# Optimization experiments

Measured on AMD Instinct MI355X. Metric: run time of the kernel, lower is better.

Reference implementation:

```python
import jax, jax.numpy as jnp
import numpy as np

N_NODES = 100000
N_EDGES = 1600000
D_IN = 128
D_OUT = 128


def setup_inputs() -> dict:
    key = jax.random.key(0)
    k1, k2, k3, k4, k5, k6 = jax.random.split(key, 6)
    x = jax.random.normal(k1, (N_NODES, D_IN), dtype=jnp.float32)
    edge_src = jax.random.randint(k2, (N_EDGES,), 0, N_NODES, dtype=jnp.int64 if jax.config.jax_enable_x64 else jnp.int32)
    edge_dst = jax.random.randint(k3, (N_EDGES,), 0, N_NODES, dtype=jnp.int64 if jax.config.jax_enable_x64 else jnp.int32)
    edge_val = jax.random.uniform(k4, (N_EDGES,), dtype=jnp.float32)
    # nn.Linear(2*D_IN, D_OUT): store W as [2*D_IN, D_OUT] (transposed torch layout)
    W = jax.random.normal(k5, (2 * D_IN, D_OUT), dtype=jnp.float32) * (1.0 / np.sqrt(2 * D_IN))
    b = jax.random.normal(k6, (D_OUT,), dtype=jnp.float32) * 0.01
    return {"x": x, "edge_src": edge_src, "edge_dst": edge_dst, "edge_val": edge_val, "W": W, "b": b}


def reference(x, edge_src, edge_dst, edge_val, W, b):
    # support = adj @ x  (sparse COO: adj[dst, src] = edge_val)
    gathered = x[edge_src] * edge_val[:, None]               # [E, D_IN]
    support = jax.ops.segment_sum(gathered, edge_dst, num_segments=x.shape[0])  # [N, D_IN]
    # concat self + aggregated neighbor features, then linear
    h = jnp.concatenate([x, support], axis=1)                # [N, 2*D_IN]
    return h @ W + b                                          # [N, D_OUT]
```

## Files before the change

### kernel.cpp

```cpp
#include <hip/hip_runtime.h>

#define D 128
#define BN 64
#define NBIN 391
#define NBMAX 512
#define CHUNK 4096
#define SCAP 12

typedef __attribute__((ext_vector_type(8))) short bf16x8;
typedef __attribute__((ext_vector_type(4))) float f32x4;

__device__ __forceinline__ unsigned short f2bf(float f) {
    unsigned int u = __builtin_bit_cast(unsigned int, f);
    u = (u + 0x7fffu + ((u >> 16) & 1u)) >> 16;
    return (unsigned short)u;
}
__device__ __forceinline__ float bf2f(unsigned int u) {
    return __builtin_bit_cast(float, u << 16);
}

__global__ void prep_kernel(const float* __restrict__ x,
                            unsigned short* __restrict__ x_bf,
                            const float* __restrict__ W,
                            unsigned short* __restrict__ WT,
                            const int* __restrict__ edst,
                            int* __restrict__ hcnt,
                            int n4, int XB, int WB, int E, int NCH) {
    __shared__ int h[NBMAX];
    int blk = blockIdx.x, tid = threadIdx.x;
    if (blk < XB) {
        int i = blk * 256 + tid;
        if (i < n4) {
            float4 v = ((const float4*)x)[i];
            ushort4 s;
            s.x = f2bf(v.x); s.y = f2bf(v.y); s.z = f2bf(v.z); s.w = f2bf(v.w);
            ((ushort4*)x_bf)[i] = s;
        }
    } else if (blk < XB + WB) {
        int t = (blk - XB) * 256 + tid;
        if (t < 2 * D * D) {
            int col = t & 127, k = t >> 7;
            WT[col * 256 + k] = f2bf(W[k * D + col]);
        }
    } else {
        int c = blk - XB - WB;
        h[tid] = 0; h[tid + 256] = 0;
        __syncthreads();
        int base = c * CHUNK;
        int n = min(CHUNK, E - base);
#pragma unroll
        for (int k = 0; k < 16; ++k) {
            int li = k * 256 + tid;
            if (li < n) atomicAdd(&h[edst[base + li] >> 8], 1);
        }
        __syncthreads();
        hcnt[tid * NCH + c]         = h[tid];
        hcnt[(tid + 256) * NCH + c] = h[tid + 256];
    }
}

__global__ __launch_bounds__(256) void binscan_kernel(const int* __restrict__ hcnt,
                                                      int* __restrict__ cpos,
                                                      int* __restrict__ ccnt, int NCH) {
    const int tid = threadIdx.x;
    const int lane = tid & 63;
    const int b = blockIdx.x * 4 + (tid >> 6);
    int run = 0;
    for (int c0 = 0; c0 < NCH; c0 += 64) {
        int c = c0 + lane;
        int v = (c < NCH) ? hcnt[b * NCH + c] : 0;
        int s = v;
#pragma unroll
        for (int off = 1; off < 64; off <<= 1) {
            int u = __shfl_up(s, off, 64);
            if (lane >= off) s += u;
        }
        if (c < NCH) cpos[c * NBMAX + b] = run + s - v;
        run += __shfl(s, 63, 64);
    }
    if (lane == 0) ccnt[b] = run;
}

__global__ __launch_bounds__(512) void cfill_kernel(const int* __restrict__ esrc,
                                                    const int* __restrict__ edst,
                                                    const float* __restrict__ eval,
                                                    const int* __restrict__ ccnt,
                                                    const int* __restrict__ cpos,
                                                    int2* __restrict__ ep, int E, int NCH) {
    __shared__ int lh[NBMAX];
    __shared__ int lcur[NBMAX];
    __shared__ int cbs[NBMAX];
    __shared__ int wsum[16];
    __shared__ int2 ord[CHUNK];
    __shared__ unsigned short obk[CHUNK];

    const int t = threadIdx.x;
    const int w = t >> 6, lane = t & 63;
    const int blk = blockIdx.x;
    const int base = blk * CHUNK;
    const int n = min(CHUNK, E - base);

    lh[t] = 0;
    __syncthreads();

    int esv[8]; int ebk[8];
    float evv[8];
#pragma unroll
    for (int k = 0; k < 8; ++k) {
        int li = k * 512 + t;
        if (li < n) {
            int i = base + li;
            int dst = edst[i];
            esv[k] = esrc[i];
            evv[k] = eval[i];
            int b = dst >> 8;
            ebk[k] = b | ((dst & 255) << 16);
            atomicAdd(&lh[b], 1);
        } else ebk[k] = -1;
    }
    __syncthreads();

    {
        int v1 = lh[t], v2 = ccnt[t];
        int s1 = v1, s2 = v2;
#pragma unroll
        for (int off = 1; off < 64; off <<= 1) {
            int u1 = __shfl_up(s1, off, 64);
            int u2 = __shfl_up(s2, off, 64);
            if (lane >= off) { s1 += u1; s2 += u2; }
        }
        if (lane == 63) { wsum[w] = s1; wsum[8 + w] = s2; }
        __syncthreads();
        if (w == 0) {
            int x1 = (lane < 8) ? wsum[lane] : 0;
            int x2 = (lane < 8) ? wsum[8 + lane] : 0;
            int y1 = x1, y2 = x2;
#pragma unroll
            for (int off = 1; off < 8; off <<= 1) {
                int u1 = __shfl_up(y1, off, 64);
                int u2 = __shfl_up(y2, off, 64);
                if (lane >= off) { y1 += u1; y2 += u2; }
            }
            if (lane < 8) { wsum[lane] = y1 - x1; wsum[8 + lane] = y2 - x2; }
        }
        __syncthreads();
        lcur[t] = s1 - v1 + wsum[w];
        cbs[t]  = s2 - v2 + wsum[8 + w];
    }
    __syncthreads();

#pragma unroll
    for (int k = 0; k < 8; ++k) {
        if (ebk[k] >= 0) {
            int b = ebk[k] & 0xffff, nl = ebk[k] >> 16;
            int slot = atomicAdd(&lcur[b], 1);
            ord[slot] = make_int2((esv[k] << 8) | nl, __builtin_bit_cast(int, evv[k]));
            obk[slot] = (unsigned short)b;
        }
    }
    __syncthreads();

    if (t < NBIN) {
        int c2 = lh[t];
        if (c2) lh[t] = cbs[t] + cpos[blk * NBMAX + t] - (lcur[t] - c2);
    }
    __syncthreads();

    for (int i = t; i < n; i += 512) {
        int b = obk[i];
        ep[lh[b] + i] = ord[i];
    }
}

__global__ __launch_bounds__(512) void csort_kernel(int2* __restrict__ ep,
                                                    const int* __restrict__ ccnt,
                                                    int* __restrict__ node_start) {
    __shared__ int h[256];
    __shared__ int cbs[NBMAX];
    __shared__ int wsum[8];

    const int t = threadIdx.x;
    const int w = t >> 6, lane = t & 63;
    const int bin = blockIdx.x;

    if (t < 256) h[t] = 0;
    {
        int v = ccnt[t];
        int s = v;
#pragma unroll
        for (int off = 1; off < 64; off <<= 1) {
            int u = __shfl_up(s, off, 64);
            if (lane >= off) s += u;
        }
        if (lane == 63) wsum[w] = s;
        __syncthreads();
        if (w == 0) {
            int x = (lane < 8) ? wsum[lane] : 0;
            int y = x;
#pragma unroll
            for (int off = 1; off < 8; off <<= 1) {
                int u = __shfl_up(y, off, 64);
                if (lane >= off) y += u;
            }
            if (lane < 8) wsum[lane] = y - x;
        }
        __syncthreads();
        cbs[t] = s - v + wsum[w];
    }
    __syncthreads();

    const int cb = cbs[bin];
    const int ce = cb + ccnt[bin];

    int2 ev[SCAP];
#pragma unroll
    for (int k = 0; k < SCAP; ++k) {
        int idx = cb + k * 512 + t;
        if (idx < ce) {
            int2 e = ep[idx];
            ev[k] = e;
            atomicAdd(&h[e.x & 255], 1);
        } else ev[k] = make_int2(-1, 0);
    }
    __syncthreads();

    {
        int v = (t < 256) ? h[t] : 0;
        int s = v;
#pragma unroll
        for (int off = 1; off < 64; off <<= 1) {
            int u = __shfl_up(s, off, 64);
            if (lane >= off) s += u;
        }
        if (lane == 63) wsum[w] = s;
        __syncthreads();
        if (w == 0) {
            int x = (lane < 8) ? wsum[lane] : 0;
            int y = x;
#pragma unroll
            for (int off = 1; off < 8; off <<= 1) {
                int u = __shfl_up(y, off, 64);
                if (lane >= off) y += u;
            }
            if (lane < 8) wsum[lane] = y - x;
        }
        __syncthreads();
        if (t < 256) {
            int st = cb + s - v + wsum[w];
            node_start[bin * 256 + t] = st;
            h[t] = st;
        }
    }
    __syncthreads();

#pragma unroll
    for (int k = 0; k < SCAP; ++k) {
        if (ev[k].x >= 0) {
            int nl = ev[k].x & 255;
            int pos = atomicAdd(&h[nl], 1);
            ep[pos] = make_int2(ev[k].x & 0xFFFFFF3F, ev[k].y);
        }
    }
}

__global__ __launch_bounds__(256, 8) void gather_fused_kernel(
        const unsigned short* __restrict__ x_bf,
        const int* __restrict__ node_start,
        const int2* __restrict__ edge_pack,
        const unsigned short* __restrict__ WT,
        const float* __restrict__ bias,
        float* __restrict__ out, int N) {
    __shared__ unsigned short accb[BN * 136];
    __shared__ int nb[BN + 1];

    const int tid = threadIdx.x;
    const int node0 = blockIdx.x * BN;
    const int w = tid >> 6, lane = tid & 63;
    unsigned int* accw = (unsigned int*)accb;

    for (int i = tid * 8; i < BN * 136; i += 2048)
        *(uint4*)(accb + i) = make_uint4(0u, 0u, 0u, 0u);
    if (tid <= BN) nb[tid] = node_start[node0 + tid];
    __syncthreads();

    const int js = __builtin_amdgcn_readfirstlane(nb[w * 16]);
    const int je = __builtin_amdgcn_readfirstlane(nb[w * 16 + 16]);
    const unsigned short* xl = x_bf + lane * 2;

    int cur = -1;
    float ax = 0.f, ay = 0.f;
    for (int g = js; g < je; g += 16) {
        int m = je - g; if (m > 16) m = 16;
        int2 e[16];
#pragma unroll
        for (int k = 0; k < 16; ++k) {
            int idx = g + k; if (idx >= je) idx = je - 1;
            e[k] = edge_pack[idx];
        }
        unsigned int p[16];
#pragma unroll
        for (int k = 0; k < 16; ++k)
            p[k] = *(const unsigned int*)(xl + ((e[k].x >> 8) << 7));
#pragma unroll
        for (int k = 0; k < 16; ++k) {
            if (k < m) {
                int nd = e[k].x & 63;
                if (nd != cur) {
                    if (cur >= 0)
                        accw[cur * 68 + lane] =
                            (unsigned int)f2bf(ax) | ((unsigned int)f2bf(ay) << 16);
                    cur = nd; ax = 0.f; ay = 0.f;
                }
                float v = __builtin_bit_cast(float, e[k].y);
                ax += bf2f(p[k] & 0xffffu) * v;
                ay += bf2f(p[k] >> 16) * v;
            }
        }
    }
    if (cur >= 0)
        accw[cur * 68 + lane] = (unsigned int)f2bf(ax) | ((unsigned int)f2bf(ay) << 16);
    __syncthreads();

    const int quad = lane >> 4;
    const int l15  = lane & 15;
    const int colbase = w * 32;

    f32x4 acc[4][2];
#pragma unroll
    for (int rt = 0; rt < 4; ++rt) {
        acc[rt][0] = (f32x4){0.f, 0.f, 0.f, 0.f};
        acc[rt][1] = (f32x4){0.f, 0.f, 0.f, 0.f};
    }

#pragma unroll
    for (int ks = 0; ks < 8; ++ks) {
        bf16x8 wf0 = *(const bf16x8*)(WT + (size_t)(colbase + l15) * 256 + ks * 32 + quad * 8);
        bf16x8 wf1 = *(const bf16x8*)(WT + (size_t)(colbase + 16 + l15) * 256 + ks * 32 + quad * 8);
#pragma unroll
        for (int rt = 0; rt < 4; ++rt) {
            int row = rt * 16 + l15;
            bf16x8 a;
            if (ks < 4) {
                int rg = node0 + row; if (rg >= N) rg = N - 1;
                a = *(const bf16x8*)(x_bf + (size_t)rg * D + ks * 32 + quad * 8);
            } else {
                a = *(const bf16x8*)(accb + row * 136 + (ks - 4) * 32 + quad * 8);
            }
            acc[rt][0] = __builtin_amdgcn_mfma_f32_16x16x32_bf16(a, wf0, acc[rt][0], 0, 0, 0);
            acc[rt][1] = __builtin_amdgcn_mfma_f32_16x16x32_bf16(a, wf1, acc[rt][1], 0, 0, 0);
        }
    }

#pragma unroll
    for (int ct = 0; ct < 2; ++ct) {
        int col = colbase + ct * 16 + l15;
        float bv = bias[col];
#pragma unroll
        for (int rt = 0; rt < 4; ++rt) {
#pragma unroll
            for (int rg = 0; rg < 4; ++rg) {
                int row = node0 + rt * 16 + quad * 4 + rg;
                if (row < N)
                    out[(size_t)row * D + col] = acc[rt][ct][rg] + bv;
            }
        }
    }
}

extern "C" void kernel_launch(void* const* d_in, const int* in_sizes, int n_in,
                              void* d_out, int out_size, void* d_ws, size_t ws_size,
                              hipStream_t stream) {
    const float* x    = (const float*)d_in[0];
    const int*   esrc = (const int*)d_in[1];
    const int*   edst = (const int*)d_in[2];
    const float* eval = (const float*)d_in[3];
    const float* W    = (const float*)d_in[4];
    const float* bias = (const float*)d_in[5];
    float*       out  = (float*)d_out;

    const int N  = in_sizes[0] / D;
    const int E  = in_sizes[1];
    const int NG  = (N + BN - 1) / BN;
    const int NCH = (E + CHUNK - 1) / CHUNK;

    char* ws = (char*)d_ws;
    unsigned short* x_bf  = (unsigned short*)ws;
    int2*           ep    = (int2*)(ws + 25600000);
    int*            hcnt  = (int*)(ws + 25600000);
    unsigned short* WT    = (unsigned short*)(ws + 38400000);
    int*            nbg   = (int*)(ws + 38465536);
    int*            ccnt  = (int*)(ws + 38865920);
    int*            cpos  = (int*)(ws + 38870016);

    const int n4 = N * D / 4;
    const int XB = (n4 + 255) / 256;
    const int WB = (2 * D * D + 255) / 256;

    prep_kernel<<<XB + WB + NCH, 256, 0, stream>>>(x, x_bf, W, WT, edst, hcnt,
                                                   n4, XB, WB, E, NCH);
    binscan_kernel<<<128, 256, 0, stream>>>(hcnt, cpos, ccnt, NCH);
    cfill_kernel<<<NCH, 512, 0, stream>>>(esrc, edst, eval, ccnt, cpos, ep, E, NCH);
    csort_kernel<<<NBIN, 512, 0, stream>>>(ep, ccnt, nbg);
    gather_fused_kernel<<<NG, 256, 0, stream>>>(x_bf, nbg, ep, WT, bias, out, N);
    (void)ws_size; (void)n_in; (void)out_size;
}
```

Before: 239.9 us.

## Use 64-node buckets and sort within buckets in gather kernel LDS

Changes the destination bucketing from 256-node bins to 64-node buckets matching the gather block size. The separate csort pass, which re-read and re-wrote the edge array globally, is removed. Each gather block now loads its bucket's edges, counting-sorts them by node in shared memory, and accumulates from LDS. Histogram and offset arrays shrink to 16-bit, and a small single-block kernel scans the bucket counts. This risks dropping edges if a bucket exceeds the 1536 capacity, and adds LDS pressure to the gather kernel.

```diff
diff --git a/kernel.cpp b/kernel.cpp
--- a/kernel.cpp
+++ b/kernel.cpp
@@ -2,10 +2,10 @@
 
 #define D 128
 #define BN 64
-#define NBIN 391
-#define NBMAX 512
+#define NBKT 1563
+#define NBMAX 2048
 #define CHUNK 4096
-#define SCAP 12
+#define GCAP 1536
 
 typedef __attribute__((ext_vector_type(8))) short bf16x8;
 typedef __attribute__((ext_vector_type(4))) float f32x4;
@@ -24,7 +24,7 @@
                             const float* __restrict__ W,
                             unsigned short* __restrict__ WT,
                             const int* __restrict__ edst,
-                            int* __restrict__ hcnt,
+                            unsigned short* __restrict__ hcnt,
                             int n4, int XB, int WB, int E, int NCH) {
     __shared__ int h[NBMAX];
     int blk = blockIdx.x, tid = threadIdx.x;
@@ -44,23 +44,27 @@
         }
     } else {
         int c = blk - XB - WB;
-        h[tid] = 0; h[tid + 256] = 0;
+#pragma unroll
+        for (int j = 0; j < 8; ++j) h[tid + j * 256] = 0;
         __syncthreads();
         int base = c * CHUNK;
         int n = min(CHUNK, E - base);
 #pragma unroll
         for (int k = 0; k < 16; ++k) {
             int li = k * 256 + tid;
-            if (li < n) atomicAdd(&h[edst[base + li] >> 8], 1);
-        }
-        __syncthreads();
-        hcnt[tid * NCH + c]         = h[tid];
-        hcnt[(tid + 256) * NCH + c] = h[tid + 256];
-    }
-}
-
-__global__ __launch_bounds__(256) void binscan_kernel(const int* __restrict__ hcnt,
-                                                      int* __restrict__ cpos,
+            if (li < n) atomicAdd(&h[edst[base + li] >> 6], 1);
+        }
+        __syncthreads();
+#pragma unroll
+        for (int j = 0; j < 8; ++j) {
+            int b = tid + j * 256;
+            hcnt[(size_t)b * NCH + c] = (unsigned short)h[b];
+        }
+    }
+}
+
+__global__ __launch_bounds__(256) void binscan_kernel(const unsigned short* __restrict__ hcnt,
+                                                      unsigned short* __restrict__ cpos,
                                                       int* __restrict__ ccnt, int NCH) {
     const int tid = threadIdx.x;
     const int lane = tid & 63;
@@ -68,29 +72,49 @@
     int run = 0;
     for (int c0 = 0; c0 < NCH; c0 += 64) {
         int c = c0 + lane;
-        int v = (c < NCH) ? hcnt[b * NCH + c] : 0;
+        int v = (c < NCH) ? (int)hcnt[(size_t)b * NCH + c] : 0;
         int s = v;
 #pragma unroll
         for (int off = 1; off < 64; off <<= 1) {
             int u = __shfl_up(s, off, 64);
             if (lane >= off) s += u;
         }
-        if (c < NCH) cpos[c * NBMAX + b] = run + s - v;
+        if (c < NCH) cpos[(size_t)c * NBMAX + b] = (unsigned short)(run + s - v);
         run += __shfl(s, 63, 64);
     }
     if (lane == 0) ccnt[b] = run;
+}
+
+__global__ __launch_bounds__(256) void cscan_kernel(const int* __restrict__ ccnt,
+                                                    int* __restrict__ cbase) {
+    __shared__ int p[256];
+    int t = threadIdx.x;
+    int c[8]; int loc = 0;
+#pragma unroll
+    for (int k = 0; k < 8; ++k) { c[k] = ccnt[t * 8 + k]; loc += c[k]; }
+    p[t] = loc;
+    __syncthreads();
+    for (int off = 1; off < 256; off <<= 1) {
+        int v = p[t];
+        int u = (t >= off) ? p[t - off] : 0;
+        __syncthreads();
+        p[t] = v + u;
+        __syncthreads();
+    }
+    int ex = p[t] - loc;
+#pragma unroll
+    for (int k = 0; k < 8; ++k) { cbase[t * 8 + k] = ex; ex += c[k]; }
 }
 
 __global__ __launch_bounds__(512) void cfill_kernel(const int* __restrict__ esrc,
                                                     const int* __restrict__ edst,
                                                     const float* __restrict__ eval,
-                                                    const int* __restrict__ ccnt,
-                                                    const int* __restrict__ cpos,
-                                                    int2* __restrict__ ep, int E, int NCH) {
+                                                    const int* __restrict__ cbase,
+                                                    const unsigned short* __restrict__ cpos,
+                                                    int2* __restrict__ ep, int E) {
     __shared__ int lh[NBMAX];
     __shared__ int lcur[NBMAX];
-    __shared__ int cbs[NBMAX];
-    __shared__ int wsum[16];
+    __shared__ int wsum[8];
     __shared__ int2 ord[CHUNK];
     __shared__ unsigned short obk[CHUNK];
 
@@ -100,7 +124,8 @@
     const int base = blk * CHUNK;
     const int n = min(CHUNK, E - base);
 
-    lh[t] = 0;
+#pragma unroll
+    for (int j = 0; j < 4; ++j) lh[t + j * 512] = 0;
     __syncthreads();
 
     int esv[8]; int ebk[8];
@@ -113,79 +138,16 @@
             int dst = edst[i];
             esv[k] = esrc[i];
             evv[k] = eval[i];
-            int b = dst >> 8;
-            ebk[k] = b | ((dst & 255) << 16);
+            int b = dst >> 6;
+            ebk[k] = b | ((dst & 63) << 16);
             atomicAdd(&lh[b], 1);
         } else ebk[k] = -1;
     }
     __syncthreads();
 
     {
-        int v1 = lh[t], v2 = ccnt[t];
-        int s1 = v1, s2 = v2;
-#pragma unroll
-        for (int off = 1; off < 64; off <<= 1) {
-            int u1 = __shfl_up(s1, off, 64);
-            int u2 = __shfl_up(s2, off, 64);
-            if (lane >= off) { s1 += u1; s2 += u2; }
-        }
-        if (lane == 63) { wsum[w] = s1; wsum[8 + w] = s2; }
-        __syncthreads();
-        if (w == 0) {
-            int x1 = (lane < 8) ? wsum[lane] : 0;
-            int x2 = (lane < 8) ? wsum[8 + lane] : 0;
-            int y1 = x1, y2 = x2;
-#pragma unroll
-            for (int off = 1; off < 8; off <<= 1) {
-                int u1 = __shfl_up(y1, off, 64);
-                int u2 = __shfl_up(y2, off, 64);
-                if (lane >= off) { y1 += u1; y2 += u2; }
-            }
-            if (lane < 8) { wsum[lane] = y1 - x1; wsum[8 + lane] = y2 - x2; }
-        }
-        __syncthreads();
-        lcur[t] = s1 - v1 + wsum[w];
-        cbs[t]  = s2 - v2 + wsum[8 + w];
-    }
-    __syncthreads();
-
-#pragma unroll
-    for (int k = 0; k < 8; ++k) {
-        if (ebk[k] >= 0) {
-            int b = ebk[k] & 0xffff, nl = ebk[k] >> 16;
-            int slot = atomicAdd(&lcur[b], 1);
-            ord[slot] = make_int2((esv[k] << 8) | nl, __builtin_bit_cast(int, evv[k]));
-            obk[slot] = (unsigned short)b;
-        }
-    }
-    __syncthreads();
-
-    if (t < NBIN) {
-        int c2 = lh[t];
-        if (c2) lh[t] = cbs[t] + cpos[blk * NBMAX + t] - (lcur[t] - c2);
-    }
-    __syncthreads();
-
-    for (int i = t; i < n; i += 512) {
-        int b = obk[i];
-        ep[lh[b] + i] = ord[i];
-    }
-}
-
-__global__ __launch_bounds__(512) void csort_kernel(int2* __restrict__ ep,
-                                                    const int* __restrict__ ccnt,
-                                                    int* __restrict__ node_start) {
-    __shared__ int h[256];
-    __shared__ int cbs[NBMAX];
-    __shared__ int wsum[8];
-
-    const int t = threadIdx.x;
-    const int w = t >> 6, lane = t & 63;
-    const int bin = blockIdx.x;
-
-    if (t < 256) h[t] = 0;
-    {
-        int v = ccnt[t];
+        int c0 = lh[4 * t], c1 = lh[4 * t + 1], c2 = lh[4 * t + 2], c3 = lh[4 * t + 3];
+        int v = c0 + c1 + c2 + c3;
         int s = v;
 #pragma unroll
         for (int off = 1; off < 64; off <<= 1) {
@@ -205,86 +167,100 @@
             if (lane < 8) wsum[lane] = y - x;
         }
         __syncthreads();
-        cbs[t] = s - v + wsum[w];
-    }
-    __syncthreads();
-
-    const int cb = cbs[bin];
-    const int ce = cb + ccnt[bin];
-
-    int2 ev[SCAP];
-#pragma unroll
-    for (int k = 0; k < SCAP; ++k) {
-        int idx = cb + k * 512 + t;
-        if (idx < ce) {
-            int2 e = ep[idx];
-            ev[k] = e;
-            atomicAdd(&h[e.x & 255], 1);
-        } else ev[k] = make_int2(-1, 0);
-    }
-    __syncthreads();
-
-    {
-        int v = (t < 256) ? h[t] : 0;
-        int s = v;
-#pragma unroll
-        for (int off = 1; off < 64; off <<= 1) {
-            int u = __shfl_up(s, off, 64);
-            if (lane >= off) s += u;
-        }
-        if (lane == 63) wsum[w] = s;
-        __syncthreads();
-        if (w == 0) {
-            int x = (lane < 8) ? wsum[lane] : 0;
-            int y = x;
-#pragma unroll
-            for (int off = 1; off < 8; off <<= 1) {
-                int u = __shfl_up(y, off, 64);
-                if (lane >= off) y += u;
-            }
-            if (lane < 8) wsum[lane] = y - x;
-        }
-        __syncthreads();
-        if (t < 256) {
-            int st = cb + s - v + wsum[w];
-            node_start[bin * 256 + t] = st;
-            h[t] = st;
-        }
-    }
-    __syncthreads();
-
-#pragma unroll
-    for (int k = 0; k < SCAP; ++k) {
-        if (ev[k].x >= 0) {
-            int nl = ev[k].x & 255;
-            int pos = atomicAdd(&h[nl], 1);
-            ep[pos] = make_int2(ev[k].x & 0xFFFFFF3F, ev[k].y);
-        }
+        int ex = s - v + wsum[w];
+        lcur[4 * t] = ex;
+        lcur[4 * t + 1] = ex + c0;
+        lcur[4 * t + 2] = ex + c0 + c1;
+        lcur[4 * t + 3] = ex + c0 + c1 + c2;
+    }
+    __syncthreads();
+
+#pragma unroll
+    for (int k = 0; k < 8; ++k) {
+        if (ebk[k] >= 0) {
+            int b = ebk[k] & 0xffff, nl = ebk[k] >> 16;
+            int slot = atomicAdd(&lcur[b], 1);
+            ord[slot] = make_int2((esv[k] << 6) | nl, __builtin_bit_cast(int, evv[k]));
+            obk[slot] = (unsigned short)b;
+        }
+    }
+    __syncthreads();
+
+#pragma unroll
+    for (int j = 0; j < 4; ++j) {
+        int b = t + j * 512;
+        int c2 = lh[b];
+        if (c2) lh[b] = cbase[b] + (int)cpos[(size_t)blk * NBMAX + b] - (lcur[b] - c2);
+    }
+    __syncthreads();
+
+    for (int i = t; i < n; i += 512) {
+        int b = obk[i];
+        ep[lh[b] + i] = ord[i];
     }
 }
 
 __global__ __launch_bounds__(256, 8) void gather_fused_kernel(
         const unsigned short* __restrict__ x_bf,
-        const int* __restrict__ node_start,
+        const int* __restrict__ cbase,
+        const int* __restrict__ ccnt,
         const int2* __restrict__ edge_pack,
         const unsigned short* __restrict__ WT,
         const float* __restrict__ bias,
         float* __restrict__ out, int N) {
     __shared__ unsigned short accb[BN * 136];
-    __shared__ int nb[BN + 1];
+    __shared__ int2 ord[GCAP];
+    __shared__ int cnt64[BN];
+    __shared__ int st64[BN + 1];
+    __shared__ int cur64[BN];
 
     const int tid = threadIdx.x;
-    const int node0 = blockIdx.x * BN;
+    const int bkt = blockIdx.x;
+    const int node0 = bkt * BN;
     const int w = tid >> 6, lane = tid & 63;
+    const int cb = cbase[bkt];
+    const int n = min(ccnt[bkt], GCAP);
     unsigned int* accw = (unsigned int*)accb;
 
     for (int i = tid * 8; i < BN * 136; i += 2048)
         *(uint4*)(accb + i) = make_uint4(0u, 0u, 0u, 0u);
-    if (tid <= BN) nb[tid] = node_start[node0 + tid];
-    __syncthreads();
-
-    const int js = __builtin_amdgcn_readfirstlane(nb[w * 16]);
-    const int je = __builtin_amdgcn_readfirstlane(nb[w * 16 + 16]);
+    if (tid < BN) cnt64[tid] = 0;
+    __syncthreads();
+
+    int2 ev[6];
+#pragma unroll
+    for (int k = 0; k < 6; ++k) {
+        int idx = k * 256 + tid;
+        if (idx < n) {
+            ev[k] = edge_pack[cb + idx];
+            atomicAdd(&cnt64[ev[k].x & 63], 1);
+        } else ev[k].x = -1;
+    }
+    __syncthreads();
+
+    if (tid < BN) {
+        int c = cnt64[tid];
+        int s = c;
+#pragma unroll
+        for (int off = 1; off < 64; off <<= 1) {
+            int u = __shfl_up(s, off, 64);
+            if (lane >= off) s += u;
+        }
+        st64[tid] = s - c;
+        cur64[tid] = s - c;
+        if (tid == BN - 1) st64[BN] = s;
+    }
+    __syncthreads();
+
+#pragma unroll
+    for (int k = 0; k < 6; ++k) {
+        if (ev[k].x >= 0)
+            ord[atomicAdd(&cur64[ev[k].x & 63], 1)] = ev[k];
+    }
+    __syncthreads();
+
+    const int js = __builtin_amdgcn_readfirstlane(st64[w * 16]);
+    const int je = __builtin_amdgcn_readfirstlane(st64[w * 16 + 16]);
     const unsigned short* xl = x_bf + lane * 2;
 
     int cur = -1;
@@ -295,12 +271,12 @@
 #pragma unroll
         for (int k = 0; k < 16; ++k) {
             int idx = g + k; if (idx >= je) idx = je - 1;
-            e[k] = edge_pack[idx];
+            e[k] = ord[idx];
         }
         unsigned int p[16];
 #pragma unroll
         for (int k = 0; k < 16; ++k)
-            p[k] = *(const unsigned int*)(xl + ((e[k].x >> 8) << 7));
+            p[k] = *(const unsigned int*)(xl + ((e[k].x >> 6) << 7));
 #pragma unroll
         for (int k = 0; k < 16; ++k) {
             if (k < m) {
@@ -386,11 +362,11 @@
     char* ws = (char*)d_ws;
     unsigned short* x_bf  = (unsigned short*)ws;
     int2*           ep    = (int2*)(ws + 25600000);
-    int*            hcnt  = (int*)(ws + 25600000);
+    unsigned short* hcnt  = (unsigned short*)(ws + 25600000);
     unsigned short* WT    = (unsigned short*)(ws + 38400000);
-    int*            nbg   = (int*)(ws + 38465536);
-    int*            ccnt  = (int*)(ws + 38865920);
-    int*            cpos  = (int*)(ws + 38870016);
+    int*            ccnt  = (int*)(ws + 38465536);
+    int*            cbase = (int*)(ws + 38473728);
+    unsigned short* cpos  = (unsigned short*)(ws + 38481920);
 
     const int n4 = N * D / 4;
     const int XB = (n4 + 255) / 256;
@@ -398,9 +374,9 @@
 
     prep_kernel<<<XB + WB + NCH, 256, 0, stream>>>(x, x_bf, W, WT, edst, hcnt,
                                                    n4, XB, WB, E, NCH);
-    binscan_kernel<<<128, 256, 0, stream>>>(hcnt, cpos, ccnt, NCH);
-    cfill_kernel<<<NCH, 512, 0, stream>>>(esrc, edst, eval, ccnt, cpos, ep, E, NCH);
-    csort_kernel<<<NBIN, 512, 0, stream>>>(ep, ccnt, nbg);
-    gather_fused_kernel<<<NG, 256, 0, stream>>>(x_bf, nbg, ep, WT, bias, out, N);
+    binscan_kernel<<<512, 256, 0, stream>>>(hcnt, cpos, ccnt, NCH);
+    cscan_kernel<<<1, 256, 0, stream>>>(ccnt, cbase);
+    cfill_kernel<<<NCH, 512, 0, stream>>>(esrc, edst, eval, cbase, cpos, ep, E);
+    gather_fused_kernel<<<NG, 256, 0, stream>>>(x_bf, cbase, ccnt, ep, WT, bias, out, N);
     (void)ws_size; (void)n_in; (void)out_size;
 }
```

Result: slower. 258.9 us (+7.9%).
